# Performance work log

Measured on AMD Instinct MI355X. Metric: run time of the kernel, lower is better.

The kernel has to match this reference:

```python
import jax, jax.numpy as jnp
import numpy as np

ALPHA = 0.2          # LeakyReLU negative slope
NEG_INF = -9e15      # matches torch's -9000000000000000.0 mask value


def _gat_layer(x, adj_mask, W, a1, a2, concat):
    """One GraphAttentionLayerBatch (eval mode, dropout off).

    The original builds a_input = [h_i || h_j] of shape [B,N,N,2F] and dots
    with a = [a1; a2]; that is mathematically the separable score
    a1.h_i + a2.h_j, which we compute directly without the O(N^2*2F) tensor.
    """
    h = jnp.einsum('bnf,fo->bno', x, W)            # [B, N, F_out]
    f1 = jnp.einsum('bno,o->bn', h, a1)            # a1 . h_i
    f2 = jnp.einsum('bno,o->bn', h, a2)            # a2 . h_j
    e = jax.nn.leaky_relu(f1[:, :, None] + f2[:, None, :], negative_slope=ALPHA)
    e = jnp.where(adj_mask, e, NEG_INF)            # [B, N, N]
    att = jax.nn.softmax(e, axis=2)
    h_prime = jnp.einsum('bnm,bmo->bno', att, h)   # [B, N, F_out]
    return jax.nn.elu(h_prime) if concat else h_prime


def setup_inputs() -> dict:
    key = jax.random.key(0)
    ks = jax.random.split(key, 9)
    B, N, nfeat, nhid, nclass, H = 32, 512, 128, 64, 16, 8
    x = jax.random.normal(ks[0], (B, N, nfeat), dtype=jnp.float32)
    adj = jax.random.randint(ks[1], (B, N, N), 0, 2, dtype=jnp.int32)
    W_heads = jax.random.normal(ks[2], (H, nfeat, nhid), dtype=jnp.float32) * 0.1
    a1_heads = jax.random.normal(ks[3], (H, nhid), dtype=jnp.float32) * 0.1
    a2_heads = jax.random.normal(ks[4], (H, nhid), dtype=jnp.float32) * 0.1
    W_out = jax.random.normal(ks[5], (nhid * H, nclass), dtype=jnp.float32) * 0.05
    a1_out = jax.random.normal(ks[6], (nclass,), dtype=jnp.float32) * 0.1
    a2_out = jax.random.normal(ks[7], (nclass,), dtype=jnp.float32) * 0.1
    return {"x": x, "adj": adj, "W_heads": W_heads, "a1_heads": a1_heads,
            "a2_heads": a2_heads, "W_out": W_out, "a1_out": a1_out,
            "a2_out": a2_out}


def reference(x, adj, W_heads, a1_heads, a2_heads, W_out, a1_out, a2_out):
    mask = adj > 0  # [B, N, N]
    # multi-head attention layers (concat=True)
    heads = jax.vmap(lambda W, a1, a2: _gat_layer(x, mask, W, a1, a2, True))(
        W_heads, a1_heads, a2_heads)              # [H, B, N, nhid]
    H, B, N, F = heads.shape
    x_cat = jnp.transpose(heads, (1, 2, 0, 3)).reshape(B, N, H * F)
    # output attention layer (concat=False)
    return _gat_layer(x_cat, mask, W_out, a1_out, a2_out, False)
```

## Files before the change

kernel.cpp:

```cpp
#include <hip/hip_runtime.h>
#include <hip/hip_bf16.h>

#define GB 32
#define GN 512
#define GFIN 128
#define GFH 64
#define GH 8
#define GC 16

typedef short short8 __attribute__((ext_vector_type(8)));
typedef float f32x4 __attribute__((ext_vector_type(4)));

__device__ __forceinline__ ushort f2bf(float f) {
  unsigned u = __float_as_uint(f);
  return (ushort)((u + 0x7FFFu + ((u >> 16) & 1u)) >> 16);
}
__device__ __forceinline__ unsigned pk2(float a, float b) {
  float2 f2; f2.x = a; f2.y = b;
  __hip_bfloat162 h = __float22bfloat162_rn(f2);
  union { __hip_bfloat162 h; unsigned u; } cv;
  cv.h = h;
  return cv.u;
}
__device__ __forceinline__ short8 ones8() {
  short8 o;
#pragma unroll
  for (int i = 0; i < 8; ++i) o[i] = (short)0x3F80;
  return o;
}

__global__ __launch_bounds__(256) void k_pack_gemm1(
    const int* __restrict__ adj, unsigned* __restrict__ mw,
    const float* __restrict__ xg, const float* __restrict__ Wg,
    const float* __restrict__ a1g, const float* __restrict__ a2g,
    ushort* __restrict__ VTg, float* __restrict__ f1g, float* __restrict__ f2g,
    const float* __restrict__ Wog, ushort* __restrict__ WoT) {
  __shared__ ushort Wt[64][136];
  __shared__ ushort xl[128][136];
  int blk = blockIdx.x;
  int tid = threadIdx.x;

  if (blk == 5120) {
    for (int i = tid; i < 512 * GC; i += 256) {
      int k = i & 511, cc = i >> 9;
      WoT[cc * 512 + k] = f2bf(Wog[(size_t)k * GC + cc]);
    }
    return;
  }
  if (blk >= 1024) {
    int pblk = blk - 1024;
    int lane = tid & 63;
    int base = pblk * 2048 + tid;
    int v[8];
#pragma unroll
    for (int it = 0; it < 8; ++it) v[it] = adj[(size_t)base + it * 256];
#pragma unroll
    for (int it = 0; it < 8; ++it) {
      unsigned long long m = __ballot(v[it] > 0);
      int idx = base + it * 256;
      if (lane == 0)       mw[idx >> 5] = (unsigned)m;
      else if (lane == 32) mw[idx >> 5] = (unsigned)(m >> 32);
    }
    return;
  }

  int bh = blk >> 2, rq = blk & 3;
  int b = bh >> 3, h = bh & 7;
  int r0 = rq * 128;
  int lane = tid & 63, w = tid >> 6;
  int c = lane & 15, q = lane >> 4;

  const float* Wh = Wg + (size_t)h * GFIN * GFH;
  for (int i = tid; i < GFIN * GFH; i += 256) {
    int f = i >> 6, j = i & 63;
    Wt[j][f] = f2bf(Wh[i]);
  }
  const float* xb = xg + ((size_t)b * GN + r0) * GFIN;
  for (int u = tid; u < 128 * 32; u += 256) {
    int row = u >> 5, c4 = u & 31;
    float4 xf = *(const float4*)&xb[(size_t)row * GFIN + c4 * 4];
    uint2 us;
    us.x = pk2(xf.x, xf.y);
    us.y = pk2(xf.z, xf.w);
    *(uint2*)&xl[row][c4 * 4] = us;
  }
  __syncthreads();

  short8 Bf[4][4];
#pragma unroll
  for (int cb = 0; cb < 4; ++cb)
#pragma unroll
    for (int kk = 0; kk < 4; ++kk)
      Bf[cb][kk] = *(const short8*)&Wt[cb * 16 + c][kk * 32 + q * 8];

  float a1v[4], a2v[4];
#pragma unroll
  for (int cb = 0; cb < 4; ++cb) {
    a1v[cb] = a1g[h * 64 + cb * 16 + c];
    a2v[cb] = a2g[h * 64 + cb * 16 + c];
  }

  f32x4 acc[2][4];
#pragma unroll
  for (int r = 0; r < 2; ++r)
#pragma unroll
    for (int cb = 0; cb < 4; ++cb) acc[r][cb] = (f32x4){0.f, 0.f, 0.f, 0.f};

#pragma unroll
  for (int kk = 0; kk < 4; ++kk) {
    short8 A0 = *(const short8*)&xl[(w * 2 + 0) * 16 + c][kk * 32 + q * 8];
    short8 A1 = *(const short8*)&xl[(w * 2 + 1) * 16 + c][kk * 32 + q * 8];
#pragma unroll
    for (int cb = 0; cb < 4; ++cb) {
      acc[0][cb] = __builtin_amdgcn_mfma_f32_16x16x32_bf16(A0, Bf[cb][kk], acc[0][cb], 0, 0, 0);
      acc[1][cb] = __builtin_amdgcn_mfma_f32_16x16x32_bf16(A1, Bf[cb][kk], acc[1][cb], 0, 0, 0);
    }
  }

  ushort* VT = VTg + (size_t)bh * GN * GFH;
  float* f1o = f1g + (size_t)bh * GN;
  float* f2o = f2g + (size_t)bh * GN;
#pragma unroll
  for (int rbi = 0; rbi < 2; ++rbi) {
    int rowb = r0 + (w * 2 + rbi) * 16 + q * 4;
    float v1[4] = {0.f, 0.f, 0.f, 0.f}, v2[4] = {0.f, 0.f, 0.f, 0.f};
#pragma unroll
    for (int cb = 0; cb < 4; ++cb) {
      f32x4 a = acc[rbi][cb];
      uint2 vs;
      vs.x = pk2(a[0], a[1]);
      vs.y = pk2(a[2], a[3]);
      *(uint2*)&VT[(size_t)(cb * 16 + c) * GN + rowb] = vs;
#pragma unroll
      for (int i = 0; i < 4; ++i) {
        v1[i] += a[i] * a1v[cb];
        v2[i] += a[i] * a2v[cb];
      }
    }
#pragma unroll
    for (int i = 0; i < 4; ++i) {
#pragma unroll
      for (int off = 1; off < 16; off <<= 1) {
        v1[i] += __shfl_xor(v1[i], off);
        v2[i] += __shfl_xor(v2[i], off);
      }
      if (c == 0) { f1o[rowb + i] = v1[i]; f2o[rowb + i] = v2[i]; }
    }
  }
}

__global__ __launch_bounds__(256, 4) void k_attn1(
    const ushort* __restrict__ VTg, const unsigned* __restrict__ mwg,
    const float* __restrict__ f1g, const float* __restrict__ f2g,
    ushort* __restrict__ xcb) {
  __shared__ ushort P[32][520];
  int blk = blockIdx.x;
  int bh = blk & 255, rq = blk >> 8;
  int b = bh >> 3, h = bh & 7;
  int r0 = rq * 128;
  int tid = threadIdx.x, lane = tid & 63, w = tid >> 6;
  int c = lane & 15, q = lane >> 4;

  const unsigned* mwb = mwg + (size_t)b * GN * 16;
  const float* f1w = f1g + (size_t)bh * GN;
  const float* f2w = f2g + (size_t)bh * GN;

  float4 fa = *(const float4*)&f2w[lane * 8];
  float4 fb = *(const float4*)&f2w[lane * 8 + 4];
  float E2[8], e2[8];
  {
    float f2v[8] = {fa.x, fa.y, fa.z, fa.w, fb.x, fb.y, fb.z, fb.w};
#pragma unroll
    for (int i = 0; i < 8; ++i) {
      E2[i] = __expf(f2v[i]);
      e2[i] = __expf(0.2f * f2v[i]);
    }
  }
  float f1v = 0.f;
  if (lane < 32) f1v = f1w[r0 + ((lane >> 3) << 5) + w + ((lane & 7) << 2)];
  float E1v = __expf(f1v), e1v = __expf(0.2f * f1v);

  const ushort* VT = VTg + (size_t)bh * GN * GFH + (size_t)(w * 16 + c) * GN + q * 8;
  short8 Bf[16];
#pragma unroll
  for (int kk = 0; kk < 16; ++kk) Bf[kk] = *(const short8*)&VT[kk * 32];
  const short8 ONES = ones8();

  for (int t = 0; t < 4; ++t) {
    int tb = r0 + t * 32;
    unsigned mword[8];
#pragma unroll
    for (int ri = 0; ri < 8; ++ri)
      mword[ri] = mwb[(size_t)(tb + w + 4 * ri) * 16 + (lane >> 2)];
#pragma unroll
    for (int ri = 0; ri < 8; ++ri) {
      float E1r = __shfl(E1v, t * 8 + ri);
      float e1r = __shfl(e1v, t * 8 + ri);
      unsigned mb = (mword[ri] >> (8 * (lane & 3))) & 0xffu;
      float p[8];
#pragma unroll
      for (int i = 0; i < 8; ++i) {
        float v = fmaxf(E1r * E2[i], e1r * e2[i]);
        p[i] = ((mb >> i) & 1u) ? v : 0.f;
      }
      uint4 u;
      u.x = pk2(p[0], p[1]);
      u.y = pk2(p[2], p[3]);
      u.z = pk2(p[4], p[5]);
      u.w = pk2(p[6], p[7]);
      *(uint4*)&P[w + 4 * ri][lane * 8] = u;
    }
    __syncthreads();

    f32x4 acc0 = (f32x4){0.f, 0.f, 0.f, 0.f};
    f32x4 acc1 = (f32x4){0.f, 0.f, 0.f, 0.f};
    f32x4 aL0 = (f32x4){0.f, 0.f, 0.f, 0.f};
    f32x4 aL1 = (f32x4){0.f, 0.f, 0.f, 0.f};
#pragma unroll
    for (int kk = 0; kk < 16; ++kk) {
      short8 A0 = *(const short8*)&P[c][kk * 32 + q * 8];
      short8 A1 = *(const short8*)&P[16 + c][kk * 32 + q * 8];
      acc0 = __builtin_amdgcn_mfma_f32_16x16x32_bf16(A0, Bf[kk], acc0, 0, 0, 0);
      aL0  = __builtin_amdgcn_mfma_f32_16x16x32_bf16(A0, ONES,   aL0, 0, 0, 0);
      acc1 = __builtin_amdgcn_mfma_f32_16x16x32_bf16(A1, Bf[kk], acc1, 0, 0, 0);
      aL1  = __builtin_amdgcn_mfma_f32_16x16x32_bf16(A1, ONES,   aL1, 0, 0, 0);
    }
#pragma unroll
    for (int rbi = 0; rbi < 2; ++rbi) {
      f32x4 a = rbi ? acc1 : acc0;
      f32x4 aL = rbi ? aL1 : aL0;
#pragma unroll
      for (int i = 0; i < 4; ++i) {
        int row = tb + rbi * 16 + q * 4 + i;
        float v = a[i] / fmaxf(aL[i], 1e-30f);
        v = v > 0.f ? v : __expf(v) - 1.f;
        xcb[((size_t)(b * GN + row)) * 512 + h * 64 + w * 16 + c] = f2bf(v);
      }
    }
    __syncthreads();
  }
}

__global__ __launch_bounds__(256) void k_gemm2(
    const ushort* __restrict__ xcb, const ushort* __restrict__ WoT,
    const float* __restrict__ a1g, const float* __restrict__ a2g,
    ushort* __restrict__ hTg, float* __restrict__ f1b, float* __restrict__ f2b) {
  __shared__ ushort xl[64][520];
  int b = blockIdx.x >> 3, r0 = (blockIdx.x & 7) * 64;
  int tid = threadIdx.x, lane = tid & 63, w = tid >> 6;
  int c = lane & 15, q = lane >> 4;

  const ushort* xb = xcb + ((size_t)b * GN + r0) * 512;
  for (int i = tid; i < 64 * 64; i += 256) {
    int row = i >> 6, c8 = i & 63;
    *(uint4*)&xl[row][c8 * 8] = *(const uint4*)&xb[(size_t)row * 512 + c8 * 8];
  }
  short8 Bf[16];
#pragma unroll
  for (int kk = 0; kk < 16; ++kk)
    Bf[kk] = *(const short8*)&WoT[(size_t)c * 512 + kk * 32 + q * 8];
  __syncthreads();

  f32x4 acc = (f32x4){0.f, 0.f, 0.f, 0.f};
#pragma unroll
  for (int kk = 0; kk < 16; ++kk) {
    short8 A = *(const short8*)&xl[w * 16 + c][kk * 32 + q * 8];
    acc = __builtin_amdgcn_mfma_f32_16x16x32_bf16(A, Bf[kk], acc, 0, 0, 0);
  }

  float a1v = a1g[c], a2v = a2g[c];
  int rowb = r0 + w * 16 + q * 4;
  uint2 vs;
  vs.x = pk2(acc[0], acc[1]);
  vs.y = pk2(acc[2], acc[3]);
  *(uint2*)&hTg[((size_t)b * GC + c) * 512 + rowb] = vs;
#pragma unroll
  for (int i = 0; i < 4; ++i) {
    float v1 = acc[i] * a1v, v2 = acc[i] * a2v;
#pragma unroll
    for (int off = 1; off < 16; off <<= 1) {
      v1 += __shfl_xor(v1, off);
      v2 += __shfl_xor(v2, off);
    }
    if (c == 0) {
      f1b[(size_t)b * GN + rowb + i] = v1;
      f2b[(size_t)b * GN + rowb + i] = v2;
    }
  }
}

__global__ __launch_bounds__(256) void k_attn2(
    const ushort* __restrict__ hTg, const unsigned* __restrict__ mwg,
    const float* __restrict__ f1g, const float* __restrict__ f2g,
    float* __restrict__ outg) {
  __shared__ ushort P[64][520];
  int b = blockIdx.x >> 3, r0 = (blockIdx.x & 7) * 64;
  int tid = threadIdx.x, lane = tid & 63, w = tid >> 6;
  int c = lane & 15, q = lane >> 4;

  const unsigned* mwb = mwg + (size_t)b * GN * 16;
  const float* f1w = f1g + (size_t)b * GN;
  const float* f2w = f2g + (size_t)b * GN;

  float4 fa = *(const float4*)&f2w[lane * 8];
  float4 fb = *(const float4*)&f2w[lane * 8 + 4];
  float E2[8], e2[8];
  {
    float f2v[8] = {fa.x, fa.y, fa.z, fa.w, fb.x, fb.y, fb.z, fb.w};
#pragma unroll
    for (int i = 0; i < 8; ++i) {
      E2[i] = __expf(f2v[i]);
      e2[i] = __expf(0.2f * f2v[i]);
    }
  }
  float f1v = 0.f;
  if (lane < 16) f1v = f1w[r0 + w * 16 + lane];
  float E1v = __expf(f1v), e1v = __expf(0.2f * f1v);

  short8 Bf[16];
#pragma unroll
  for (int kk = 0; kk < 16; ++kk)
    Bf[kk] = *(const short8*)&hTg[((size_t)b * GC + c) * 512 + kk * 32 + q * 8];
  const short8 ONES = ones8();

  unsigned mword[16];
#pragma unroll
  for (int ri = 0; ri < 16; ++ri)
    mword[ri] = mwb[(size_t)(r0 + w * 16 + ri) * 16 + (lane >> 2)];

#pragma unroll
  for (int ri = 0; ri < 16; ++ri) {
    float E1r = __shfl(E1v, ri);
    float e1r = __shfl(e1v, ri);
    unsigned mb = (mword[ri] >> (8 * (lane & 3))) & 0xffu;
    float p[8];
#pragma unroll
    for (int i = 0; i < 8; ++i) {
      float v = fmaxf(E1r * E2[i], e1r * e2[i]);
      p[i] = ((mb >> i) & 1u) ? v : 0.f;
    }
    uint4 u;
    u.x = pk2(p[0], p[1]);
    u.y = pk2(p[2], p[3]);
    u.z = pk2(p[4], p[5]);
    u.w = pk2(p[6], p[7]);
    *(uint4*)&P[w * 16 + ri][lane * 8] = u;
  }
  __syncthreads();

  f32x4 acc = (f32x4){0.f, 0.f, 0.f, 0.f};
  f32x4 aL = (f32x4){0.f, 0.f, 0.f, 0.f};
#pragma unroll
  for (int kk = 0; kk < 16; ++kk) {
    short8 A = *(const short8*)&P[w * 16 + c][kk * 32 + q * 8];
    acc = __builtin_amdgcn_mfma_f32_16x16x32_bf16(A, Bf[kk], acc, 0, 0, 0);
    aL  = __builtin_amdgcn_mfma_f32_16x16x32_bf16(A, ONES, aL, 0, 0, 0);
  }
#pragma unroll
  for (int i = 0; i < 4; ++i) {
    int row = r0 + w * 16 + q * 4 + i;
    outg[((size_t)(b * GN + row)) * GC + c] = acc[i] / fmaxf(aL[i], 1e-30f);
  }
}

extern "C" void kernel_launch(void* const* d_in, const int* in_sizes, int n_in,
                              void* d_out, int out_size, void* d_ws, size_t ws_size,
                              hipStream_t stream) {
  (void)in_sizes; (void)n_in; (void)out_size;
  const float* x   = (const float*)d_in[0];
  const int*   adj = (const int*)d_in[1];
  const float* Whd = (const float*)d_in[2];
  const float* a1h = (const float*)d_in[3];
  const float* a2h = (const float*)d_in[4];
  const float* Wo  = (const float*)d_in[5];
  const float* a1o = (const float*)d_in[6];
  const float* a2o = (const float*)d_in[7];

  size_t off = 0;
  char* base = (char*)d_ws;
  unsigned* mw = (unsigned*)(base + off); off += (size_t)GB * GN * 16 * 4;
  ushort* VT   = (ushort*)(base + off);   off += (size_t)GB * GH * GN * GFH * 2;
  ushort* xcb  = (ushort*)(base + off);   off += (size_t)GB * GN * 512 * 2;
  ushort* WoT  = (ushort*)(base + off);   off += (size_t)GC * 512 * 2;
  ushort* hT   = (ushort*)(base + off);   off += (size_t)GB * GC * GN * 2;
  float* f1    = (float*)(base + off);    off += (size_t)GB * GH * GN * 4;
  float* f2    = (float*)(base + off);    off += (size_t)GB * GH * GN * 4;
  float* f1b   = (float*)(base + off);    off += (size_t)GB * GN * 4;
  float* f2b   = (float*)(base + off);    off += (size_t)GB * GN * 4;

  if (ws_size < off) return;

  hipLaunchKernelGGL(k_pack_gemm1, dim3(5121), dim3(256), 0, stream,
                     adj, mw, x, Whd, a1h, a2h, VT, f1, f2, Wo, WoT);
  hipLaunchKernelGGL(k_attn1, dim3(1024), dim3(256), 0, stream,
                     VT, mw, f1, f2, xcb);
  hipLaunchKernelGGL(k_gemm2, dim3(GB * 8), dim3(256), 0, stream,
                     xcb, WoT, a1o, a2o, hT, f1b, f2b);
  hipLaunchKernelGGL(k_attn2, dim3(GB * 8), dim3(256), 0, stream,
                     hT, mw, f1b, f2b, (float*)d_out);
}
```

Before: 158.3 us.

## Fuse output GEMM and output attention into one tail kernel; prefetch mask words

Merges k_gemm2 and k_attn2 into a single k_tail kernel. Each block recomputes the full per-batch projection h = x_cat·W_out (all 512 rows) into shared memory, so hT, f1b and f2b no longer round-trip through global memory and one launch is removed. This costs redundant work: the 16x512x512 GEMM is repeated by all 8 blocks of a batch, and only 2 of 4 waves issue the attention MFMAs. Separately, k_attn1 now loads the next tile's adjacency mask words before the barrier, overlapping that load with the MFMA phase.

```diff
diff --git a/kernel.cpp b/kernel.cpp
--- a/kernel.cpp
+++ b/kernel.cpp
@@ -186,12 +186,13 @@
   for (int kk = 0; kk < 16; ++kk) Bf[kk] = *(const short8*)&VT[kk * 32];
   const short8 ONES = ones8();
 
+  unsigned mword[8];
+#pragma unroll
+  for (int ri = 0; ri < 8; ++ri)
+    mword[ri] = mwb[(size_t)(r0 + w + 4 * ri) * 16 + (lane >> 2)];
+
   for (int t = 0; t < 4; ++t) {
     int tb = r0 + t * 32;
-    unsigned mword[8];
-#pragma unroll
-    for (int ri = 0; ri < 8; ++ri)
-      mword[ri] = mwb[(size_t)(tb + w + 4 * ri) * 16 + (lane >> 2)];
 #pragma unroll
     for (int ri = 0; ri < 8; ++ri) {
       float E1r = __shfl(E1v, t * 8 + ri);
@@ -209,6 +210,11 @@
       u.z = pk2(p[4], p[5]);
       u.w = pk2(p[6], p[7]);
       *(uint4*)&P[w + 4 * ri][lane * 8] = u;
+    }
+    if (t < 3) {
+#pragma unroll
+      for (int ri = 0; ri < 8; ++ri)
+        mword[ri] = mwb[(size_t)(tb + 32 + w + 4 * ri) * 16 + (lane >> 2)];
     }
     __syncthreads();
 
@@ -241,71 +247,63 @@
   }
 }
 
-__global__ __launch_bounds__(256) void k_gemm2(
+__global__ __launch_bounds__(256) void k_tail(
     const ushort* __restrict__ xcb, const ushort* __restrict__ WoT,
-    const float* __restrict__ a1g, const float* __restrict__ a2g,
-    ushort* __restrict__ hTg, float* __restrict__ f1b, float* __restrict__ f2b) {
-  __shared__ ushort xl[64][520];
-  int b = blockIdx.x >> 3, r0 = (blockIdx.x & 7) * 64;
+    const float* __restrict__ a1o, const float* __restrict__ a2o,
+    const unsigned* __restrict__ mwg, float* __restrict__ outg) {
+  __shared__ ushort P[32][520];
+  __shared__ ushort hT[16][520];
+  __shared__ float f1s[512];
+  __shared__ float f2s[512];
+  int vb = blockIdx.x;
+  int b = vb >> 3, r0 = (vb & 7) * 64;
   int tid = threadIdx.x, lane = tid & 63, w = tid >> 6;
   int c = lane & 15, q = lane >> 4;
-
-  const ushort* xb = xcb + ((size_t)b * GN + r0) * 512;
-  for (int i = tid; i < 64 * 64; i += 256) {
-    int row = i >> 6, c8 = i & 63;
-    *(uint4*)&xl[row][c8 * 8] = *(const uint4*)&xb[(size_t)row * 512 + c8 * 8];
-  }
-  short8 Bf[16];
+  const short8 ONES = ones8();
+
+  short8 Bw[16];
 #pragma unroll
   for (int kk = 0; kk < 16; ++kk)
-    Bf[kk] = *(const short8*)&WoT[(size_t)c * 512 + kk * 32 + q * 8];
+    Bw[kk] = *(const short8*)&WoT[(size_t)c * 512 + kk * 32 + q * 8];
+  float a1v = a1o[c], a2v = a2o[c];
+
+#pragma unroll
+  for (int i = 0; i < 8; ++i) {
+    int t = w * 8 + i;
+    const ushort* arow = xcb + ((size_t)(b * GN + t * 16 + c)) * 512 + q * 8;
+    f32x4 acc = (f32x4){0.f, 0.f, 0.f, 0.f};
+#pragma unroll
+    for (int kk = 0; kk < 16; ++kk) {
+      short8 A = *(const short8*)&arow[kk * 32];
+      acc = __builtin_amdgcn_mfma_f32_16x16x32_bf16(A, Bw[kk], acc, 0, 0, 0);
+    }
+    int rowb = t * 16 + q * 4;
+    uint2 vs;
+    vs.x = pk2(acc[0], acc[1]);
+    vs.y = pk2(acc[2], acc[3]);
+    *(uint2*)&hT[c][rowb] = vs;
+#pragma unroll
+    for (int j = 0; j < 4; ++j) {
+      float v1 = acc[j] * a1v, v2 = acc[j] * a2v;
+#pragma unroll
+      for (int off = 1; off < 16; off <<= 1) {
+        v1 += __shfl_xor(v1, off);
+        v2 += __shfl_xor(v2, off);
+      }
+      if (c == 0) { f1s[rowb + j] = v1; f2s[rowb + j] = v2; }
+    }
+  }
   __syncthreads();
 
-  f32x4 acc = (f32x4){0.f, 0.f, 0.f, 0.f};
-#pragma unroll
-  for (int kk = 0; kk < 16; ++kk) {
-    short8 A = *(const short8*)&xl[w * 16 + c][kk * 32 + q * 8];
-    acc = __builtin_amdgcn_mfma_f32_16x16x32_bf16(A, Bf[kk], acc, 0, 0, 0);
-  }
-
-  float a1v = a1g[c], a2v = a2g[c];
-  int rowb = r0 + w * 16 + q * 4;
-  uint2 vs;
-  vs.x = pk2(acc[0], acc[1]);
-  vs.y = pk2(acc[2], acc[3]);
-  *(uint2*)&hTg[((size_t)b * GC + c) * 512 + rowb] = vs;
-#pragma unroll
-  for (int i = 0; i < 4; ++i) {
-    float v1 = acc[i] * a1v, v2 = acc[i] * a2v;
-#pragma unroll
-    for (int off = 1; off < 16; off <<= 1) {
-      v1 += __shfl_xor(v1, off);
-      v2 += __shfl_xor(v2, off);
-    }
-    if (c == 0) {
-      f1b[(size_t)b * GN + rowb + i] = v1;
-      f2b[(size_t)b * GN + rowb + i] = v2;
-    }
-  }
-}
-
-__global__ __launch_bounds__(256) void k_attn2(
-    const ushort* __restrict__ hTg, const unsigned* __restrict__ mwg,
-    const float* __restrict__ f1g, const float* __restrict__ f2g,
-    float* __restrict__ outg) {
-  __shared__ ushort P[64][520];
-  int b = blockIdx.x >> 3, r0 = (blockIdx.x & 7) * 64;
-  int tid = threadIdx.x, lane = tid & 63, w = tid >> 6;
-  int c = lane & 15, q = lane >> 4;
-
-  const unsigned* mwb = mwg + (size_t)b * GN * 16;
-  const float* f1w = f1g + (size_t)b * GN;
-  const float* f2w = f2g + (size_t)b * GN;
-
-  float4 fa = *(const float4*)&f2w[lane * 8];
-  float4 fb = *(const float4*)&f2w[lane * 8 + 4];
+  short8 Bh[16];
+#pragma unroll
+  for (int kk = 0; kk < 16; ++kk)
+    Bh[kk] = *(const short8*)&hT[c][kk * 32 + q * 8];
+
   float E2[8], e2[8];
   {
+    float4 fa = *(const float4*)&f2s[lane * 8];
+    float4 fb = *(const float4*)&f2s[lane * 8 + 4];
     float f2v[8] = {fa.x, fa.y, fa.z, fa.w, fb.x, fb.y, fb.z, fb.w};
 #pragma unroll
     for (int i = 0; i < 8; ++i) {
@@ -313,53 +311,52 @@
       e2[i] = __expf(0.2f * f2v[i]);
     }
   }
-  float f1v = 0.f;
-  if (lane < 16) f1v = f1w[r0 + w * 16 + lane];
-  float E1v = __expf(f1v), e1v = __expf(0.2f * f1v);
-
-  short8 Bf[16];
-#pragma unroll
-  for (int kk = 0; kk < 16; ++kk)
-    Bf[kk] = *(const short8*)&hTg[((size_t)b * GC + c) * 512 + kk * 32 + q * 8];
-  const short8 ONES = ones8();
-
+
+  const unsigned* mwb = mwg + (size_t)b * GN * 16;
   unsigned mword[16];
 #pragma unroll
   for (int ri = 0; ri < 16; ++ri)
-    mword[ri] = mwb[(size_t)(r0 + w * 16 + ri) * 16 + (lane >> 2)];
-
-#pragma unroll
-  for (int ri = 0; ri < 16; ++ri) {
-    float E1r = __shfl(E1v, ri);
-    float e1r = __shfl(e1v, ri);
-    unsigned mb = (mword[ri] >> (8 * (lane & 3))) & 0xffu;
-    float p[8];
-#pragma unroll
-    for (int i = 0; i < 8; ++i) {
-      float v = fmaxf(E1r * E2[i], e1r * e2[i]);
-      p[i] = ((mb >> i) & 1u) ? v : 0.f;
-    }
-    uint4 u;
-    u.x = pk2(p[0], p[1]);
-    u.y = pk2(p[2], p[3]);
-    u.z = pk2(p[4], p[5]);
-    u.w = pk2(p[6], p[7]);
-    *(uint4*)&P[w * 16 + ri][lane * 8] = u;
-  }
-  __syncthreads();
-
-  f32x4 acc = (f32x4){0.f, 0.f, 0.f, 0.f};
-  f32x4 aL = (f32x4){0.f, 0.f, 0.f, 0.f};
-#pragma unroll
-  for (int kk = 0; kk < 16; ++kk) {
-    short8 A = *(const short8*)&P[w * 16 + c][kk * 32 + q * 8];
-    acc = __builtin_amdgcn_mfma_f32_16x16x32_bf16(A, Bf[kk], acc, 0, 0, 0);
-    aL  = __builtin_amdgcn_mfma_f32_16x16x32_bf16(A, ONES, aL, 0, 0, 0);
-  }
-#pragma unroll
-  for (int i = 0; i < 4; ++i) {
-    int row = r0 + w * 16 + q * 4 + i;
-    outg[((size_t)(b * GN + row)) * GC + c] = acc[i] / fmaxf(aL[i], 1e-30f);
+    mword[ri] = mwb[(size_t)(r0 + (ri >> 3) * 32 + w + 4 * (ri & 7)) * 16 + (lane >> 2)];
+
+  for (int t2 = 0; t2 < 2; ++t2) {
+    int tb = r0 + t2 * 32;
+#pragma unroll
+    for (int ri = 0; ri < 8; ++ri) {
+      int rl = w + 4 * ri;
+      float f1r = f1s[tb + rl];
+      float E1r = __expf(f1r), e1r = __expf(0.2f * f1r);
+      unsigned mb = (mword[t2 * 8 + ri] >> (8 * (lane & 3))) & 0xffu;
+      float p[8];
+#pragma unroll
+      for (int i = 0; i < 8; ++i) {
+        float v = fmaxf(E1r * E2[i], e1r * e2[i]);
+        p[i] = ((mb >> i) & 1u) ? v : 0.f;
+      }
+      uint4 u;
+      u.x = pk2(p[0], p[1]);
+      u.y = pk2(p[2], p[3]);
+      u.z = pk2(p[4], p[5]);
+      u.w = pk2(p[6], p[7]);
+      *(uint4*)&P[rl][lane * 8] = u;
+    }
+    __syncthreads();
+
+    if (w < 2) {
+      f32x4 acc = (f32x4){0.f, 0.f, 0.f, 0.f};
+      f32x4 aL = (f32x4){0.f, 0.f, 0.f, 0.f};
+#pragma unroll
+      for (int kk = 0; kk < 16; ++kk) {
+        short8 A = *(const short8*)&P[w * 16 + c][kk * 32 + q * 8];
+        acc = __builtin_amdgcn_mfma_f32_16x16x32_bf16(A, Bh[kk], acc, 0, 0, 0);
+        aL  = __builtin_amdgcn_mfma_f32_16x16x32_bf16(A, ONES, aL, 0, 0, 0);
+      }
+#pragma unroll
+      for (int i = 0; i < 4; ++i) {
+        int row = tb + w * 16 + q * 4 + i;
+        outg[((size_t)(b * GN + row)) * GC + c] = acc[i] / fmaxf(aL[i], 1e-30f);
+      }
+    }
+    __syncthreads();
   }
 }
 
@@ -382,11 +379,8 @@
   ushort* VT   = (ushort*)(base + off);   off += (size_t)GB * GH * GN * GFH * 2;
   ushort* xcb  = (ushort*)(base + off);   off += (size_t)GB * GN * 512 * 2;
   ushort* WoT  = (ushort*)(base + off);   off += (size_t)GC * 512 * 2;
-  ushort* hT   = (ushort*)(base + off);   off += (size_t)GB * GC * GN * 2;
   float* f1    = (float*)(base + off);    off += (size_t)GB * GH * GN * 4;
   float* f2    = (float*)(base + off);    off += (size_t)GB * GH * GN * 4;
-  float* f1b   = (float*)(base + off);    off += (size_t)GB * GN * 4;
-  float* f2b   = (float*)(base + off);    off += (size_t)GB * GN * 4;
 
   if (ws_size < off) return;
 
@@ -394,8 +388,6 @@
                      adj, mw, x, Whd, a1h, a2h, VT, f1, f2, Wo, WoT);
   hipLaunchKernelGGL(k_attn1, dim3(1024), dim3(256), 0, stream,
                      VT, mw, f1, f2, xcb);
-  hipLaunchKernelGGL(k_gemm2, dim3(GB * 8), dim3(256), 0, stream,
-                     xcb, WoT, a1o, a2o, hT, f1b, f2b);
-  hipLaunchKernelGGL(k_attn2, dim3(GB * 8), dim3(256), 0, stream,
-                     hT, mw, f1b, f2b, (float*)d_out);
-}
+  hipLaunchKernelGGL(k_tail, dim3(256), dim3(256), 0, stream,
+                     xcb, WoT, a1o, a2o, mw, (float*)d_out);
+}
```

Result: slower. 182.1 us (+15.1%).

## Double-buffer attention tiles in attn1, shrink attn2 tiles, drop LDS staging in gemm2

Applied to the files above, without the earlier changes.

In k_attn1 the P tile in LDS is now double-buffered. The next tile's probabilities are computed and its mask words prefetched while the MFMA work on the current tile runs, which removes one barrier per tile. The occupancy hint drops from 4 to 2 blocks per CU because LDS use doubles. k_gemm2 now reads A fragments straight from global memory instead of staging them through shared memory, and k_attn2 uses 32-row tiles over twice as many blocks, with only two waves doing the MFMA work.

```diff
diff --git a/kernel.cpp b/kernel.cpp
--- a/kernel.cpp
+++ b/kernel.cpp
@@ -149,11 +149,11 @@
   }
 }
 
-__global__ __launch_bounds__(256, 4) void k_attn1(
+__global__ __launch_bounds__(256, 2) void k_attn1(
     const ushort* __restrict__ VTg, const unsigned* __restrict__ mwg,
     const float* __restrict__ f1g, const float* __restrict__ f2g,
     ushort* __restrict__ xcb) {
-  __shared__ ushort P[32][520];
+  __shared__ ushort P[2][32][520];
   int blk = blockIdx.x;
   int bh = blk & 255, rq = blk >> 8;
   int b = bh >> 3, h = bh & 7;
@@ -186,31 +186,37 @@
   for (int kk = 0; kk < 16; ++kk) Bf[kk] = *(const short8*)&VT[kk * 32];
   const short8 ONES = ones8();
 
+  unsigned mn[8];
+#pragma unroll
+  for (int ri = 0; ri < 8; ++ri)
+    mn[ri] = mwb[(size_t)(r0 + w + 4 * ri) * 16 + (lane >> 2)];
+#pragma unroll
+  for (int ri = 0; ri < 8; ++ri) {
+    float E1r = __shfl(E1v, ri);
+    float e1r = __shfl(e1v, ri);
+    unsigned mb = (mn[ri] >> (8 * (lane & 3))) & 0xffu;
+    float p[8];
+#pragma unroll
+    for (int i = 0; i < 8; ++i) {
+      float v = fmaxf(E1r * E2[i], e1r * e2[i]);
+      p[i] = ((mb >> i) & 1u) ? v : 0.f;
+    }
+    uint4 u;
+    u.x = pk2(p[0], p[1]);
+    u.y = pk2(p[2], p[3]);
+    u.z = pk2(p[4], p[5]);
+    u.w = pk2(p[6], p[7]);
+    *(uint4*)&P[0][w + 4 * ri][lane * 8] = u;
+  }
+#pragma unroll
+  for (int ri = 0; ri < 8; ++ri)
+    mn[ri] = mwb[(size_t)(r0 + 32 + w + 4 * ri) * 16 + (lane >> 2)];
+  __syncthreads();
+
+#pragma unroll
   for (int t = 0; t < 4; ++t) {
     int tb = r0 + t * 32;
-    unsigned mword[8];
-#pragma unroll
-    for (int ri = 0; ri < 8; ++ri)
-      mword[ri] = mwb[(size_t)(tb + w + 4 * ri) * 16 + (lane >> 2)];
-#pragma unroll
-    for (int ri = 0; ri < 8; ++ri) {
-      float E1r = __shfl(E1v, t * 8 + ri);
-      float e1r = __shfl(e1v, t * 8 + ri);
-      unsigned mb = (mword[ri] >> (8 * (lane & 3))) & 0xffu;
-      float p[8];
-#pragma unroll
-      for (int i = 0; i < 8; ++i) {
-        float v = fmaxf(E1r * E2[i], e1r * e2[i]);
-        p[i] = ((mb >> i) & 1u) ? v : 0.f;
-      }
-      uint4 u;
-      u.x = pk2(p[0], p[1]);
-      u.y = pk2(p[2], p[3]);
-      u.z = pk2(p[4], p[5]);
-      u.w = pk2(p[6], p[7]);
-      *(uint4*)&P[w + 4 * ri][lane * 8] = u;
-    }
-    __syncthreads();
+    const ushort (*Pc)[520] = P[t & 1];
 
     f32x4 acc0 = (f32x4){0.f, 0.f, 0.f, 0.f};
     f32x4 acc1 = (f32x4){0.f, 0.f, 0.f, 0.f};
@@ -218,13 +224,40 @@
     f32x4 aL1 = (f32x4){0.f, 0.f, 0.f, 0.f};
 #pragma unroll
     for (int kk = 0; kk < 16; ++kk) {
-      short8 A0 = *(const short8*)&P[c][kk * 32 + q * 8];
-      short8 A1 = *(const short8*)&P[16 + c][kk * 32 + q * 8];
+      short8 A0 = *(const short8*)&Pc[c][kk * 32 + q * 8];
+      short8 A1 = *(const short8*)&Pc[16 + c][kk * 32 + q * 8];
       acc0 = __builtin_amdgcn_mfma_f32_16x16x32_bf16(A0, Bf[kk], acc0, 0, 0, 0);
       aL0  = __builtin_amdgcn_mfma_f32_16x16x32_bf16(A0, ONES,   aL0, 0, 0, 0);
       acc1 = __builtin_amdgcn_mfma_f32_16x16x32_bf16(A1, Bf[kk], acc1, 0, 0, 0);
       aL1  = __builtin_amdgcn_mfma_f32_16x16x32_bf16(A1, ONES,   aL1, 0, 0, 0);
     }
+
+    if (t < 3) {
+#pragma unroll
+      for (int ri = 0; ri < 8; ++ri) {
+        float E1r = __shfl(E1v, (t + 1) * 8 + ri);
+        float e1r = __shfl(e1v, (t + 1) * 8 + ri);
+        unsigned mb = (mn[ri] >> (8 * (lane & 3))) & 0xffu;
+        float p[8];
+#pragma unroll
+        for (int i = 0; i < 8; ++i) {
+          float v = fmaxf(E1r * E2[i], e1r * e2[i]);
+          p[i] = ((mb >> i) & 1u) ? v : 0.f;
+        }
+        uint4 u;
+        u.x = pk2(p[0], p[1]);
+        u.y = pk2(p[2], p[3]);
+        u.z = pk2(p[4], p[5]);
+        u.w = pk2(p[6], p[7]);
+        *(uint4*)&P[(t + 1) & 1][w + 4 * ri][lane * 8] = u;
+      }
+      if (t < 2) {
+#pragma unroll
+        for (int ri = 0; ri < 8; ++ri)
+          mn[ri] = mwb[(size_t)(tb + 64 + w + 4 * ri) * 16 + (lane >> 2)];
+      }
+    }
+
 #pragma unroll
     for (int rbi = 0; rbi < 2; ++rbi) {
       f32x4 a = rbi ? acc1 : acc0;
@@ -243,32 +276,28 @@
 
 __global__ __launch_bounds__(256) void k_gemm2(
     const ushort* __restrict__ xcb, const ushort* __restrict__ WoT,
-    const float* __restrict__ a1g, const float* __restrict__ a2g,
-    ushort* __restrict__ hTg, float* __restrict__ f1b, float* __restrict__ f2b) {
-  __shared__ ushort xl[64][520];
-  int b = blockIdx.x >> 3, r0 = (blockIdx.x & 7) * 64;
+    const float* __restrict__ a1o, const float* __restrict__ a2o,
+    ushort* __restrict__ hTg, float* __restrict__ f1bg,
+    float* __restrict__ f2bg) {
+  int vb = blockIdx.x;
+  int b = vb >> 3, r0 = (vb & 7) * 64;
   int tid = threadIdx.x, lane = tid & 63, w = tid >> 6;
   int c = lane & 15, q = lane >> 4;
 
-  const ushort* xb = xcb + ((size_t)b * GN + r0) * 512;
-  for (int i = tid; i < 64 * 64; i += 256) {
-    int row = i >> 6, c8 = i & 63;
-    *(uint4*)&xl[row][c8 * 8] = *(const uint4*)&xb[(size_t)row * 512 + c8 * 8];
-  }
   short8 Bf[16];
 #pragma unroll
   for (int kk = 0; kk < 16; ++kk)
     Bf[kk] = *(const short8*)&WoT[(size_t)c * 512 + kk * 32 + q * 8];
-  __syncthreads();
-
+
+  const ushort* xrow = xcb + ((size_t)(b * GN + r0 + w * 16 + c)) * 512 + q * 8;
   f32x4 acc = (f32x4){0.f, 0.f, 0.f, 0.f};
 #pragma unroll
   for (int kk = 0; kk < 16; ++kk) {
-    short8 A = *(const short8*)&xl[w * 16 + c][kk * 32 + q * 8];
+    short8 A = *(const short8*)&xrow[kk * 32];
     acc = __builtin_amdgcn_mfma_f32_16x16x32_bf16(A, Bf[kk], acc, 0, 0, 0);
   }
 
-  float a1v = a1g[c], a2v = a2g[c];
+  float a1v = a1o[c], a2v = a2o[c];
   int rowb = r0 + w * 16 + q * 4;
   uint2 vs;
   vs.x = pk2(acc[0], acc[1]);
@@ -283,8 +312,8 @@
       v2 += __shfl_xor(v2, off);
     }
     if (c == 0) {
-      f1b[(size_t)b * GN + rowb + i] = v1;
-      f2b[(size_t)b * GN + rowb + i] = v2;
+      f1bg[(size_t)b * GN + rowb + i] = v1;
+      f2bg[(size_t)b * GN + rowb + i] = v2;
     }
   }
 }
@@ -293,10 +322,12 @@
     const ushort* __restrict__ hTg, const unsigned* __restrict__ mwg,
     const float* __restrict__ f1g, const float* __restrict__ f2g,
     float* __restrict__ outg) {
-  __shared__ ushort P[64][520];
-  int b = blockIdx.x >> 3, r0 = (blockIdx.x & 7) * 64;
+  __shared__ ushort P[32][520];
+  int vb = blockIdx.x;
+  int b = vb >> 4, r0 = (vb & 15) * 32;
   int tid = threadIdx.x, lane = tid & 63, w = tid >> 6;
   int c = lane & 15, q = lane >> 4;
+  const short8 ONES = ones8();
 
   const unsigned* mwb = mwg + (size_t)b * GN * 16;
   const float* f1w = f1g + (size_t)b * GN;
@@ -314,22 +345,15 @@
     }
   }
   float f1v = 0.f;
-  if (lane < 16) f1v = f1w[r0 + w * 16 + lane];
+  if (lane < 8) f1v = f1w[r0 + w * 8 + lane];
   float E1v = __expf(f1v), e1v = __expf(0.2f * f1v);
 
-  short8 Bf[16];
-#pragma unroll
-  for (int kk = 0; kk < 16; ++kk)
-    Bf[kk] = *(const short8*)&hTg[((size_t)b * GC + c) * 512 + kk * 32 + q * 8];
-  const short8 ONES = ones8();
-
-  unsigned mword[16];
-#pragma unroll
-  for (int ri = 0; ri < 16; ++ri)
-    mword[ri] = mwb[(size_t)(r0 + w * 16 + ri) * 16 + (lane >> 2)];
-
-#pragma unroll
-  for (int ri = 0; ri < 16; ++ri) {
+  unsigned mword[8];
+#pragma unroll
+  for (int ri = 0; ri < 8; ++ri)
+    mword[ri] = mwb[(size_t)(r0 + w * 8 + ri) * 16 + (lane >> 2)];
+#pragma unroll
+  for (int ri = 0; ri < 8; ++ri) {
     float E1r = __shfl(E1v, ri);
     float e1r = __shfl(e1v, ri);
     unsigned mb = (mword[ri] >> (8 * (lane & 3))) & 0xffu;
@@ -344,22 +368,28 @@
     u.y = pk2(p[2], p[3]);
     u.z = pk2(p[4], p[5]);
     u.w = pk2(p[6], p[7]);
-    *(uint4*)&P[w * 16 + ri][lane * 8] = u;
+    *(uint4*)&P[w * 8 + ri][lane * 8] = u;
   }
   __syncthreads();
 
-  f32x4 acc = (f32x4){0.f, 0.f, 0.f, 0.f};
-  f32x4 aL = (f32x4){0.f, 0.f, 0.f, 0.f};
-#pragma unroll
-  for (int kk = 0; kk < 16; ++kk) {
-    short8 A = *(const short8*)&P[w * 16 + c][kk * 32 + q * 8];
-    acc = __builtin_amdgcn_mfma_f32_16x16x32_bf16(A, Bf[kk], acc, 0, 0, 0);
-    aL  = __builtin_amdgcn_mfma_f32_16x16x32_bf16(A, ONES, aL, 0, 0, 0);
-  }
-#pragma unroll
-  for (int i = 0; i < 4; ++i) {
-    int row = r0 + w * 16 + q * 4 + i;
-    outg[((size_t)(b * GN + row)) * GC + c] = acc[i] / fmaxf(aL[i], 1e-30f);
+  if (w < 2) {
+    short8 Bf[16];
+#pragma unroll
+    for (int kk = 0; kk < 16; ++kk)
+      Bf[kk] = *(const short8*)&hTg[((size_t)b * GC + c) * 512 + kk * 32 + q * 8];
+    f32x4 acc = (f32x4){0.f, 0.f, 0.f, 0.f};
+    f32x4 aL = (f32x4){0.f, 0.f, 0.f, 0.f};
+#pragma unroll
+    for (int kk = 0; kk < 16; ++kk) {
+      short8 A = *(const short8*)&P[w * 16 + c][kk * 32 + q * 8];
+      acc = __builtin_amdgcn_mfma_f32_16x16x32_bf16(A, Bf[kk], acc, 0, 0, 0);
+      aL  = __builtin_amdgcn_mfma_f32_16x16x32_bf16(A, ONES, aL, 0, 0, 0);
+    }
+#pragma unroll
+    for (int i = 0; i < 4; ++i) {
+      int row = r0 + w * 16 + q * 4 + i;
+      outg[((size_t)(b * GN + row)) * GC + c] = acc[i] / fmaxf(aL[i], 1e-30f);
+    }
   }
 }
 
@@ -394,8 +424,8 @@
                      adj, mw, x, Whd, a1h, a2h, VT, f1, f2, Wo, WoT);
   hipLaunchKernelGGL(k_attn1, dim3(1024), dim3(256), 0, stream,
                      VT, mw, f1, f2, xcb);
-  hipLaunchKernelGGL(k_gemm2, dim3(GB * 8), dim3(256), 0, stream,
+  hipLaunchKernelGGL(k_gemm2, dim3(256), dim3(256), 0, stream,
                      xcb, WoT, a1o, a2o, hT, f1b, f2b);
-  hipLaunchKernelGGL(k_attn2, dim3(GB * 8), dim3(256), 0, stream,
+  hipLaunchKernelGGL(k_attn2, dim3(512), dim3(256), 0, stream,
                      hT, mw, f1b, f2b, (float*)d_out);
 }
```

Result: no change. 155.2 us (-1.9%).
